# Kernel tuning notes

Hardware: AMD Instinct MI355X
Metric: run time of the kernel (lower is better)

Reference implementation:

```python
import jax, jax.numpy as jnp
import numpy as np

N0 = 1373      # hardcoded node-type split in the original forward
TAO = 0.4
EPS = 1e-12


def _l2norm(x, axis):
    # matches torch F.normalize(p=2): x / max(||x||, eps)
    n = jnp.sqrt(jnp.sum(x * x, axis=axis, keepdims=True))
    return x / jnp.maximum(n, EPS)


def setup_inputs() -> dict:
    key = jax.random.key(0)
    ks = jax.random.split(key, 12)
    N, E, D_IN, F, H, D = 20000, 320000, 256, 32, 8, 32
    feat = jax.random.normal(ks[0], (N, D_IN), jnp.float32)
    sloc = jax.random.normal(ks[1], (N, D), jnp.float32)
    topo_fea = jax.random.normal(ks[2], (N, D), jnp.float32)
    src = jax.random.randint(ks[3], (E,), 0, N)
    dst = jax.random.randint(ks[4], (E,), 0, N)
    e_feat = jax.random.randint(ks[5], (E,), 0, 4)
    s = 1.0 / np.sqrt(D_IN)
    W_proj0 = jax.random.normal(ks[6], (D_IN, H * F), jnp.float32) * s
    W_proj1 = jax.random.normal(ks[7], (D_IN, H * F), jnp.float32) * s
    W_prob = jax.random.normal(ks[8], (H, F, F), jnp.float32) * (1.0 / np.sqrt(F))
    W_res0 = jax.random.normal(ks[9], (D_IN, H * F), jnp.float32) * s
    W_res1 = jax.random.normal(ks[10], (D_IN, H * F), jnp.float32) * s
    etype_attn = jnp.ones((4,), jnp.float32)
    return dict(feat=feat, sloc=sloc, topo_fea=topo_fea, src=src, dst=dst,
                e_feat=e_feat, W_proj0=W_proj0, W_proj1=W_proj1, W_prob=W_prob,
                W_res0=W_res0, W_res1=W_res1, etype_attn=etype_attn)


def reference(feat, sloc, topo_fea, src, dst, e_feat,
              W_proj0, W_proj1, W_prob, W_res0, W_res1, etype_attn):
    N = feat.shape[0]
    H, F = W_prob.shape[0], W_prob.shape[2]
    sloc3 = sloc[:, None, :]        # (N,1,D) -- .unsqueeze(1)
    topo3 = topo_fea[:, None, :]

    # per-type node projection
    feat_src = jnp.concatenate(
        [feat[:N0] @ W_proj0, feat[N0:] @ W_proj1], axis=0).reshape(N, H, F)
    # per-head attention feature: softmax(tanh(fc4prob_i(.)), dim=feat)
    ft_attn = jax.nn.softmax(
        jnp.tanh(jnp.einsum('nhf,hfg->nhg', feat_src, W_prob)), axis=2)
    # F.normalize over the NODE dimension (dim=0), as in original
    ft_norm = _l2norm(feat_src, axis=0)

    sloc_n = _l2norm(sloc3, axis=2)
    topo_n = _l2norm(topo3, axis=2)

    # edge attention scores
    a = jnp.sum(ft_attn[dst] * ft_norm[src], axis=2, keepdims=True)   # (E,H,1)
    cos_s = jnp.sum(sloc_n[src] * sloc_n[dst], axis=2, keepdims=True)  # (E,1,1)
    cos_t = jnp.sum(topo_n[src] * topo_n[dst], axis=2, keepdims=True)
    sim = (TAO * cos_s + (1.0 - TAO) * cos_t + 1.0) / 2.0             # (E,1,1)
    e = (sim * a * etype_attn[e_feat][:, None, None])[:, :, 0]        # (E,H)

    # edge softmax: segment softmax over incoming edges of each dst node
    m = jax.ops.segment_max(e, dst, num_segments=N)                   # (N,H)
    ex = jnp.exp(e - m[dst])
    z = jax.ops.segment_sum(ex, dst, num_segments=N)
    att = ex / z[dst]                                                 # (E,H)

    # three u_mul_e + sum aggregations
    aw = att[:, :, None]                                              # (E,H,1)
    rst = jax.ops.segment_sum(feat_src[src] * aw, dst, num_segments=N)  # (N,H,F)
    sl2 = jax.ops.segment_sum(sloc3[src] * aw, dst, num_segments=N)     # (N,H,D)
    tp2 = jax.ops.segment_sum(topo3[src] * aw, dst, num_segments=N)     # (N,H,D)

    resval = jnp.concatenate(
        [feat[:N0] @ W_res0, feat[N0:] @ W_res1], axis=0).reshape(N, H, F)
    out_fea = jax.nn.relu(rst + resval).mean(axis=1)   # (N,F)
    out_sloc = (sl2 + sloc3).mean(axis=1)              # (N,D)
    out_topo = (tp2 + topo3).mean(axis=1)              # (N,D)
    return out_fea, out_sloc, out_topo
```

## Files before the change

kernel.cpp:

```cpp
#include <hip/hip_runtime.h>
#include <math.h>

#define HN0 1373
#define BM 128
#define BN 128
#define BK 32
#define LDT 40

typedef __attribute__((ext_vector_type(8))) short short8;
typedef __attribute__((ext_vector_type(4))) float f32x4;

__device__ inline unsigned short f2bf(float f) {
  unsigned int u = __float_as_uint(f);
  unsigned int r = (u + 0x7FFFu + ((u >> 16) & 1u)) >> 16;
  return (unsigned short)r;
}
__device__ inline float bflo(unsigned int u) { return __uint_as_float(u << 16); }
__device__ inline float bfhi(unsigned int u) { return __uint_as_float(u & 0xFFFF0000u); }

__device__ inline uint4 pack8bf(float4 a, float4 b) {
  uint4 o;
  o.x = (unsigned)f2bf(a.x) | ((unsigned)f2bf(a.y) << 16);
  o.y = (unsigned)f2bf(a.z) | ((unsigned)f2bf(a.w) << 16);
  o.z = (unsigned)f2bf(b.x) | ((unsigned)f2bf(b.y) << 16);
  o.w = (unsigned)f2bf(b.z) | ((unsigned)f2bf(b.w) << 16);
  return o;
}

__global__ __launch_bounds__(256) void prep(
    const float* __restrict__ Wp0, const float* __restrict__ Wr0,
    const float* __restrict__ Wp1, const float* __restrict__ Wr1,
    unsigned short* __restrict__ BTw,
    const float* __restrict__ sloc, const float* __restrict__ topo,
    float* __restrict__ inv_s, float* __restrict__ inv_t,
    unsigned short* __restrict__ slt,
    const int* __restrict__ dst, int* __restrict__ deg, int N, int E) {
  int b = blockIdx.x;
  int tid = threadIdx.x;
  int nodeBlocks = (N + 7) / 8;
  if (b < 1024) {
    int n = b & 511, g = b >> 9;
    const float* W;
    if (g == 0) W = (n < 256) ? Wp0 : Wr0;
    else        W = (n < 256) ? Wp1 : Wr1;
    int c = n & 255;
    BTw[(size_t)g * 512 * 256 + (size_t)n * 256 + tid] = f2bf(W[(size_t)tid * 256 + c]);
  } else if (b < 1024 + nodeBlocks) {
    int node = (b - 1024) * 8 + (tid >> 5);
    int d = tid & 31;
    if (node >= N) return;
    float s = sloc[(size_t)node * 32 + d];
    float t = topo[(size_t)node * 32 + d];
    float ss = s * s, tt = t * t;
#pragma unroll
    for (int m = 16; m >= 1; m >>= 1) {
      ss += __shfl_xor(ss, m);
      tt += __shfl_xor(tt, m);
    }
    if (d == 0) {
      inv_s[node] = 1.f / fmaxf(sqrtf(ss), 1e-12f);
      inv_t[node] = 1.f / fmaxf(sqrtf(tt), 1e-12f);
    }
    slt[(size_t)node * 64 + d] = f2bf(s);
    slt[(size_t)node * 64 + 32 + d] = f2bf(t);
  } else {
    int e = (b - 1024 - nodeBlocks) * 256 + tid;
    if (e < E) atomicAdd(&deg[dst[e]], 1);
  }
}

__global__ __launch_bounds__(256) void gemm_mfma(
    const float* __restrict__ A, const unsigned short* __restrict__ BTw,
    unsigned short* __restrict__ feat_bf, unsigned short* __restrict__ resval,
    int N) {
  __shared__ __align__(16) unsigned short As[BM * LDT];
  __shared__ __align__(16) unsigned short Bs[BN * LDT];
  int tid = threadIdx.x;
  int lane = tid & 63;
  int w = tid >> 6;
  int wr = w >> 1, wc = w & 1;

  int g0t = (HN0 + BM - 1) / BM;
  int bx = blockIdx.x;
  bool g1 = bx >= g0t;
  int rowBase = g1 ? HN0 + (bx - g0t) * BM : bx * BM;
  int rowEnd = g1 ? N : HN0;
  const unsigned short* BT = BTw + (g1 ? (size_t)512 * 256 : 0);
  int colBase = blockIdx.y * BN;

  int r0 = tid >> 2;
  int kp = (tid & 3) << 3;
  int ar1 = min(rowBase + r0, rowEnd - 1);
  int ar2 = min(rowBase + r0 + 64, rowEnd - 1);
  const float* aP1 = A + (size_t)ar1 * 256 + kp;
  const float* aP2 = A + (size_t)ar2 * 256 + kp;
  const unsigned short* bP1 = BT + (size_t)(colBase + r0) * 256 + kp;
  const unsigned short* bP2 = bP1 + (size_t)64 * 256;
  int wo1 = r0 * LDT + kp;
  int wo2 = (r0 + 64) * LDT + kp;

  int q = lane >> 4;
  int fr = lane & 15;
  int aOff = (wr * 64 + fr) * LDT + q * 8;
  int bOff = (wc * 64 + fr) * LDT + q * 8;

  f32x4 acc[4][4] = {};

  float4 fa1a = *reinterpret_cast<const float4*>(aP1);
  float4 fa1b = *reinterpret_cast<const float4*>(aP1 + 4);
  float4 fa2a = *reinterpret_cast<const float4*>(aP2);
  float4 fa2b = *reinterpret_cast<const float4*>(aP2 + 4);
  uint4 rb1 = *reinterpret_cast<const uint4*>(bP1);
  uint4 rb2 = *reinterpret_cast<const uint4*>(bP2);

  for (int t = 0; t < 8; ++t) {
    *reinterpret_cast<uint4*>(&As[wo1]) = pack8bf(fa1a, fa1b);
    *reinterpret_cast<uint4*>(&As[wo2]) = pack8bf(fa2a, fa2b);
    *reinterpret_cast<uint4*>(&Bs[wo1]) = rb1;
    *reinterpret_cast<uint4*>(&Bs[wo2]) = rb2;
    __syncthreads();
    if (t < 7) {
      int ko = (t + 1) * BK;
      fa1a = *reinterpret_cast<const float4*>(aP1 + ko);
      fa1b = *reinterpret_cast<const float4*>(aP1 + ko + 4);
      fa2a = *reinterpret_cast<const float4*>(aP2 + ko);
      fa2b = *reinterpret_cast<const float4*>(aP2 + ko + 4);
      rb1 = *reinterpret_cast<const uint4*>(bP1 + ko);
      rb2 = *reinterpret_cast<const uint4*>(bP2 + ko);
    }
    short8 af[4], bf4[4];
#pragma unroll
    for (int i = 0; i < 4; ++i) {
      af[i] = *reinterpret_cast<const short8*>(&As[aOff + i * 16 * LDT]);
      bf4[i] = *reinterpret_cast<const short8*>(&Bs[bOff + i * 16 * LDT]);
    }
#pragma unroll
    for (int i = 0; i < 4; ++i)
#pragma unroll
      for (int j = 0; j < 4; ++j)
        acc[i][j] = __builtin_amdgcn_mfma_f32_16x16x32_bf16(af[i], bf4[j], acc[i][j], 0, 0, 0);
    __syncthreads();
  }

  unsigned short* outp = (colBase < 256) ? feat_bf : resval;
  int cOff = colBase & 255;
#pragma unroll
  for (int i = 0; i < 4; ++i) {
    int rb = rowBase + wr * 64 + i * 16 + q * 4;
#pragma unroll
    for (int j = 0; j < 4; ++j) {
      int col = cOff + wc * 64 + j * 16 + fr;
      f32x4 v = acc[i][j];
#pragma unroll
      for (int rr = 0; rr < 4; ++rr) {
        int r = rb + rr;
        if (r < rowEnd) outp[(size_t)r * 256 + col] = f2bf(v[rr]);
      }
    }
  }
}

__global__ __launch_bounds__(256) void attn_probs(
    const unsigned short* __restrict__ feat_bf, const float* __restrict__ W_prob,
    unsigned short* __restrict__ ft_attn, float* __restrict__ col_ss, int N) {
  __shared__ float WL[8192];
  __shared__ float fsL[16 * 256];
  int tid = threadIdx.x;
  for (int i = tid; i < 8192; i += 256) WL[i] = W_prob[i];
  int nodeBase = blockIdx.x * 16;
  float ssp = 0.f;
  for (int i = 0; i < 16; ++i) {
    int n = nodeBase + i;
    float v = (n < N) ? __uint_as_float((unsigned)feat_bf[(size_t)n * 256 + tid] << 16) : 0.f;
    fsL[i * 256 + tid] = v;
    ssp += v * v;
  }
  atomicAdd(&col_ss[tid], ssp);
  __syncthreads();
  int h = tid >> 5, g = tid & 31;
  for (int i = 0; i < 16; ++i) {
    int n = nodeBase + i;
    if (n >= N) break;
    float t = 0.f;
    const float* wp = &WL[h * 1024 + g];
    const float* fr = &fsL[i * 256 + h * 32];
#pragma unroll
    for (int f = 0; f < 32; ++f) t = fmaf(fr[f], wp[f * 32], t);
    t = tanhf(t);
    float mx = t;
#pragma unroll
    for (int s = 16; s >= 1; s >>= 1) mx = fmaxf(mx, __shfl_xor(mx, s));
    float ex = __expf(t - mx);
    float sm = ex;
#pragma unroll
    for (int s = 16; s >= 1; s >>= 1) sm += __shfl_xor(sm, s);
    ft_attn[(size_t)n * 256 + tid] = f2bf(ex / sm);
  }
}

__global__ __launch_bounds__(512) void scan_block(const int* __restrict__ deg,
                                                  int* __restrict__ start,
                                                  int* __restrict__ bsum, int n) {
  __shared__ int buf[512];
  int tid = threadIdx.x;
  int gid = blockIdx.x * 512 + tid;
  int v = (gid < n) ? deg[gid] : 0;
  buf[tid] = v;
  __syncthreads();
  for (int off = 1; off < 512; off <<= 1) {
    int t = (tid >= off) ? buf[tid - off] : 0;
    __syncthreads();
    buf[tid] += t;
    __syncthreads();
  }
  if (gid < n) start[gid] = buf[tid] - v;
  if (tid == 511) bsum[blockIdx.x] = buf[511];
}

__global__ __launch_bounds__(256) void mid_small(float* __restrict__ col_ss,
                                                 int* __restrict__ bsum, int nb) {
  int tid = threadIdx.x;
  col_ss[tid] = 1.f / fmaxf(sqrtf(col_ss[tid]), 1e-12f);
  __shared__ int buf[128];
  if (tid < nb) buf[tid] = bsum[tid];
  __syncthreads();
  if (tid == 0) {
    int run = 0;
    for (int i = 0; i < nb; ++i) { int v = buf[i]; buf[i] = run; run += v; }
  }
  __syncthreads();
  if (tid < nb) bsum[tid] = buf[tid];
}

__global__ __launch_bounds__(256) void fill_sim(
    const int* __restrict__ src, const int* __restrict__ dst,
    const int* __restrict__ e_feat, const float* __restrict__ etype_attn,
    const unsigned short* __restrict__ slt,
    const float* __restrict__ inv_s, const float* __restrict__ inv_t,
    const int* __restrict__ start, const int* __restrict__ bsum,
    int* __restrict__ cursor, int2* __restrict__ csr, int E) {
  int tid = threadIdx.x;
  int j = tid & 7;
  int e = blockIdx.x * 32 + (tid >> 3);
  if (e >= E) return;
  int s = src[e], d = dst[e];
  const unsigned short* ps = slt + (size_t)s * 64 + j * 4;
  const unsigned short* pd = slt + (size_t)d * 64 + j * 4;
  uint2 sa = *reinterpret_cast<const uint2*>(ps);
  uint2 sb = *reinterpret_cast<const uint2*>(pd);
  uint2 ta = *reinterpret_cast<const uint2*>(ps + 32);
  uint2 tb = *reinterpret_cast<const uint2*>(pd + 32);
  float cs = bflo(sa.x) * bflo(sb.x) + bfhi(sa.x) * bfhi(sb.x) +
             bflo(sa.y) * bflo(sb.y) + bfhi(sa.y) * bfhi(sb.y);
  float ct = bflo(ta.x) * bflo(tb.x) + bfhi(ta.x) * bfhi(tb.x) +
             bflo(ta.y) * bflo(tb.y) + bfhi(ta.y) * bfhi(tb.y);
#pragma unroll
  for (int m = 4; m >= 1; m >>= 1) {
    cs += __shfl_xor(cs, m);
    ct += __shfl_xor(ct, m);
  }
  if (j == 0) {
    cs *= inv_s[s] * inv_s[d];
    ct *= inv_t[s] * inv_t[d];
    float sim = (0.4f * cs + 0.6f * ct + 1.f) * 0.5f;
    float wv = sim * etype_attn[e_feat[e]];
    int pos = start[d] + bsum[d >> 9] + atomicAdd(&cursor[d], 1);
    csr[pos] = make_int2(s, __float_as_int(wv));
  }
}

#define LOADIDX(K, V, W)                                                       \
  do {                                                                         \
    int2 c_ = csr[s0 + (K)];                                                   \
    V = c_.x;                                                                  \
    W = __int_as_float(c_.y);                                                  \
  } while (0)

#define GATHER(V, FP, SL, TP)                                                  \
  do {                                                                         \
    FP = *reinterpret_cast<const uint2*>(feat_bf + (size_t)(V) * 256 + fb);    \
    const unsigned short* sp_ = slt + (size_t)(V) * 64 + db;                   \
    SL = *reinterpret_cast<const uint2*>(sp_);                                 \
    TP = *reinterpret_cast<const uint2*>(sp_ + 32);                            \
  } while (0)

#define CONSUME(W, FP, SL, TP)                                                 \
  do {                                                                         \
    float fs0 = bflo(FP.x), fs1 = bfhi(FP.x);                                  \
    float fs2 = bflo(FP.y), fs3 = bfhi(FP.y);                                  \
    float pa = ai4.x * fs0 + ai4.y * fs1 + ai4.z * fs2 + ai4.w * fs3;          \
    pa += __shfl_xor(pa, 1);                                                   \
    pa += __shfl_xor(pa, 2);                                                   \
    pa += __shfl_xor(pa, 4);                                                   \
    float p = __expf(pa * (W));                                                \
    l += p;                                                                    \
    accf.x = fmaf(p, fs0, accf.x); accf.y = fmaf(p, fs1, accf.y);              \
    accf.z = fmaf(p, fs2, accf.z); accf.w = fmaf(p, fs3, accf.w);              \
    accs.x = fmaf(p, bflo(SL.x), accs.x); accs.y = fmaf(p, bfhi(SL.x), accs.y);\
    accs.z = fmaf(p, bflo(SL.y), accs.z); accs.w = fmaf(p, bfhi(SL.y), accs.w);\
    acct.x = fmaf(p, bflo(TP.x), acct.x); acct.y = fmaf(p, bfhi(TP.x), acct.y);\
    acct.z = fmaf(p, bflo(TP.y), acct.z); acct.w = fmaf(p, bfhi(TP.y), acct.w);\
  } while (0)

__global__ __launch_bounds__(128) void edge_aggregate(
    const unsigned short* __restrict__ feat_bf, const unsigned short* __restrict__ resval,
    const unsigned short* __restrict__ ft_attn, const float* __restrict__ inv_cn,
    const unsigned short* __restrict__ slt,
    const float* __restrict__ sloc, const float* __restrict__ topo,
    const int* __restrict__ start, const int* __restrict__ bsum,
    const int* __restrict__ deg, const int2* __restrict__ csr,
    float* __restrict__ out, int N) {
  int wave = threadIdx.x >> 6;
  int n = blockIdx.x * 2 + wave;
  if (n >= N) return;
  int lane = threadIdx.x & 63;
  int j = lane & 7;
  int fb = (lane >> 3) * 32 + j * 4;
  int db = j * 4;

  uint2 at2 = *reinterpret_cast<const uint2*>(ft_attn + (size_t)n * 256 + fb);
  float4 icn4 = *reinterpret_cast<const float4*>(inv_cn + fb);
  float4 ai4 = make_float4(bflo(at2.x) * icn4.x, bfhi(at2.x) * icn4.y,
                           bflo(at2.y) * icn4.z, bfhi(at2.y) * icn4.w);
  float l = 0.f;
  float4 accf = make_float4(0.f, 0.f, 0.f, 0.f);
  float4 accs = make_float4(0.f, 0.f, 0.f, 0.f);
  float4 acct = make_float4(0.f, 0.f, 0.f, 0.f);
  int s0 = start[n] + bsum[n >> 9];
  int dg = deg[n];

  int vA = 0, vB = 0, vC = 0;
  float wA = 0.f, wB = 0.f, wC = 0.f;
  uint2 fpA = make_uint2(0u, 0u), fpB = make_uint2(0u, 0u), fpC = make_uint2(0u, 0u);
  uint2 slA = make_uint2(0u, 0u), slB = make_uint2(0u, 0u), slC = make_uint2(0u, 0u);
  uint2 tpA = make_uint2(0u, 0u), tpB = make_uint2(0u, 0u), tpC = make_uint2(0u, 0u);
  if (dg > 0) { LOADIDX(0, vA, wA); GATHER(vA, fpA, slA, tpA); }
  if (dg > 1) { LOADIDX(1, vB, wB); GATHER(vB, fpB, slB, tpB); }
  if (dg > 2) { LOADIDX(2, vC, wC); GATHER(vC, fpC, slC, tpC); }
  int i = 0;
  for (; i + 2 < dg; i += 3) {
    CONSUME(wA, fpA, slA, tpA);
    if (i + 3 < dg) { LOADIDX(i + 3, vA, wA); GATHER(vA, fpA, slA, tpA); }
    CONSUME(wB, fpB, slB, tpB);
    if (i + 4 < dg) { LOADIDX(i + 4, vB, wB); GATHER(vB, fpB, slB, tpB); }
    CONSUME(wC, fpC, slC, tpC);
    if (i + 5 < dg) { LOADIDX(i + 5, vC, wC); GATHER(vC, fpC, slC, tpC); }
  }
  if (i < dg) CONSUME(wA, fpA, slA, tpA);
  if (i + 1 < dg) CONSUME(wB, fpB, slB, tpB);

  float invl = (l > 0.f) ? 1.f / l : 0.f;

  uint2 res2 = *reinterpret_cast<const uint2*>(resval + (size_t)n * 256 + fb);
  float4 of = make_float4(fmaxf(fmaf(accf.x, invl, bflo(res2.x)), 0.f),
                          fmaxf(fmaf(accf.y, invl, bfhi(res2.x)), 0.f),
                          fmaxf(fmaf(accf.z, invl, bflo(res2.y)), 0.f),
                          fmaxf(fmaf(accf.w, invl, bfhi(res2.y)), 0.f));
  float4 os = make_float4(accs.x * invl, accs.y * invl, accs.z * invl, accs.w * invl);
  float4 ot = make_float4(acct.x * invl, acct.y * invl, acct.z * invl, acct.w * invl);
#pragma unroll
  for (int msk = 8; msk <= 32; msk <<= 1) {
    of.x += __shfl_xor(of.x, msk); of.y += __shfl_xor(of.y, msk);
    of.z += __shfl_xor(of.z, msk); of.w += __shfl_xor(of.w, msk);
    os.x += __shfl_xor(os.x, msk); os.y += __shfl_xor(os.y, msk);
    os.z += __shfl_xor(os.z, msk); os.w += __shfl_xor(os.w, msk);
    ot.x += __shfl_xor(ot.x, msk); ot.y += __shfl_xor(ot.y, msk);
    ot.z += __shfl_xor(ot.z, msk); ot.w += __shfl_xor(ot.w, msk);
  }
  if (lane < 8) {
    float4 sln = *reinterpret_cast<const float4*>(sloc + (size_t)n * 32 + db);
    float4 tpn = *reinterpret_cast<const float4*>(topo + (size_t)n * 32 + db);
    float4 o0 = make_float4(of.x * 0.125f, of.y * 0.125f, of.z * 0.125f, of.w * 0.125f);
    float4 o1 = make_float4(fmaf(os.x, 0.125f, sln.x), fmaf(os.y, 0.125f, sln.y),
                            fmaf(os.z, 0.125f, sln.z), fmaf(os.w, 0.125f, sln.w));
    float4 o2 = make_float4(fmaf(ot.x, 0.125f, tpn.x), fmaf(ot.y, 0.125f, tpn.y),
                            fmaf(ot.z, 0.125f, tpn.z), fmaf(ot.w, 0.125f, tpn.w));
    *reinterpret_cast<float4*>(out + (size_t)n * 32 + db) = o0;
    *reinterpret_cast<float4*>(out + (size_t)N * 32 + (size_t)n * 32 + db) = o1;
    *reinterpret_cast<float4*>(out + (size_t)2 * N * 32 + (size_t)n * 32 + db) = o2;
  }
}

extern "C" void kernel_launch(void* const* d_in, const int* in_sizes, int n_in,
                              void* d_out, int out_size, void* d_ws, size_t ws_size,
                              hipStream_t stream) {
  const float* feat = (const float*)d_in[0];
  const float* sloc = (const float*)d_in[1];
  const float* topo = (const float*)d_in[2];
  const int* src = (const int*)d_in[3];
  const int* dst = (const int*)d_in[4];
  const int* e_feat = (const int*)d_in[5];
  const float* W_proj0 = (const float*)d_in[6];
  const float* W_proj1 = (const float*)d_in[7];
  const float* W_prob = (const float*)d_in[8];
  const float* W_res0 = (const float*)d_in[9];
  const float* W_res1 = (const float*)d_in[10];
  const float* etype_attn = (const float*)d_in[11];
  int E = in_sizes[3];
  int N = in_sizes[1] / 32;
  float* out = (float*)d_out;

  char* ws = (char*)d_ws;
  size_t off = 0;
  auto alloc = [&](size_t bytes) -> char* {
    char* p = ws + off;
    off += (bytes + 255) & ~(size_t)255;
    return p;
  };
  int* deg = (int*)alloc((size_t)N * 4);
  int* cursor = (int*)alloc((size_t)N * 4);
  float* col_ss = (float*)alloc(256 * 4);
  size_t zeroBytes = ((char*)col_ss + 256 * 4) - (char*)deg;
  int* startArr = (int*)alloc(((size_t)N + 1) * 4);
  int* bsum = (int*)alloc(128 * 4);
  float* inv_s = (float*)alloc((size_t)N * 4);
  float* inv_t = (float*)alloc((size_t)N * 4);
  int2* csr = (int2*)alloc((size_t)E * 8);
  unsigned short* feat_bf = (unsigned short*)alloc((size_t)N * 256 * 2);
  unsigned short* slt = (unsigned short*)alloc((size_t)N * 64 * 2);
  unsigned short* resval = (unsigned short*)alloc((size_t)N * 256 * 2);
  unsigned short* ft_attn = (unsigned short*)alloc((size_t)N * 256 * 2);
  unsigned short* BTw = (unsigned short*)alloc((size_t)2 * 512 * 256 * 2);

  hipMemsetAsync(deg, 0, zeroBytes, stream);

  int nodeBlocks = (N + 7) / 8;
  int degBlocks = (E + 255) / 256;
  prep<<<1024 + nodeBlocks + degBlocks, 256, 0, stream>>>(
      W_proj0, W_res0, W_proj1, W_res1, BTw, sloc, topo, inv_s, inv_t, slt,
      dst, deg, N, E);

  int g0t = (HN0 + BM - 1) / BM;
  int g1t = (N - HN0 + BM - 1) / BM;
  gemm_mfma<<<dim3(g0t + g1t, 4), 256, 0, stream>>>(feat, BTw, feat_bf, resval, N);

  attn_probs<<<(N + 15) / 16, 256, 0, stream>>>(feat_bf, W_prob, ft_attn, col_ss, N);

  int nb = (N + 511) / 512;
  scan_block<<<nb, 512, 0, stream>>>(deg, startArr, bsum, N);
  mid_small<<<1, 256, 0, stream>>>(col_ss, bsum, nb);

  fill_sim<<<(E + 31) / 32, 256, 0, stream>>>(src, dst, e_feat, etype_attn, slt,
                                              inv_s, inv_t, startArr, bsum,
                                              cursor, csr, E);

  edge_aggregate<<<(N + 1) / 2, 128, 0, stream>>>(feat_bf, resval, ft_attn, col_ss,
                                                  slt, sloc, topo, startArr, bsum,
                                                  deg, csr, out, N);
}
```

Before: 190.2 us.

## Tile weight transpose, prenormalize sloc/topo, register W_prob, cheaper tanh softmax

The weight transpose in prep now uses 64x64 shared-memory tiles with vectorized loads and stores, replacing 1024 blocks of strided scalar reads. Prep also writes pre-normalized bf16 sloc/topo (sltn), so fill_sim only does a weighted dot product over 16-wide vector loads with four lanes per edge and no inv_s/inv_t gathers. attn_probs keeps W_prob in registers instead of shared memory. It computes tanh through exp and a fast reciprocal, and drops the max subtraction because tanh output is bounded. These trade extra bf16 rounding of normalized values and approximate tanh and reciprocal for fewer memory passes and less arithmetic.

```diff
diff --git a/kernel.cpp b/kernel.cpp
--- a/kernel.cpp
+++ b/kernel.cpp
@@ -32,21 +32,46 @@
     const float* __restrict__ Wp1, const float* __restrict__ Wr1,
     unsigned short* __restrict__ BTw,
     const float* __restrict__ sloc, const float* __restrict__ topo,
-    float* __restrict__ inv_s, float* __restrict__ inv_t,
-    unsigned short* __restrict__ slt,
+    unsigned short* __restrict__ slt, unsigned short* __restrict__ sltn,
     const int* __restrict__ dst, int* __restrict__ deg, int N, int E) {
+  __shared__ float T[64][72];
   int b = blockIdx.x;
   int tid = threadIdx.x;
   int nodeBlocks = (N + 7) / 8;
-  if (b < 1024) {
-    int n = b & 511, g = b >> 9;
-    const float* W;
-    if (g == 0) W = (n < 256) ? Wp0 : Wr0;
-    else        W = (n < 256) ? Wp1 : Wr1;
-    int c = n & 255;
-    BTw[(size_t)g * 512 * 256 + (size_t)n * 256 + tid] = f2bf(W[(size_t)tid * 256 + c]);
-  } else if (b < 1024 + nodeBlocks) {
-    int node = (b - 1024) * 8 + (tid >> 5);
+  if (b < 64) {
+    int mat = b >> 4;
+    int t16 = b & 15;
+    int kT = (t16 & 3) * 64;
+    int nT = (t16 >> 2) * 64;
+    const float* W = (mat == 0) ? Wp0 : (mat == 1) ? Wr0 : (mat == 2) ? Wp1 : Wr1;
+    int g = mat >> 1;
+    int nbase = (mat & 1) * 256;
+    int r = tid >> 2;
+    int cb = (tid & 3) * 16;
+    const float* srcp = W + (size_t)(kT + r) * 256 + nT + cb;
+#pragma unroll
+    for (int q = 0; q < 4; ++q) {
+      float4 v = *reinterpret_cast<const float4*>(srcp + q * 4);
+      T[cb + q * 4 + 0][r] = v.x;
+      T[cb + q * 4 + 1][r] = v.y;
+      T[cb + q * 4 + 2][r] = v.z;
+      T[cb + q * 4 + 3][r] = v.w;
+    }
+    __syncthreads();
+    int nl = tid >> 2;
+    int kb = (tid & 3) * 16;
+    unsigned int pk[8];
+#pragma unroll
+    for (int q = 0; q < 8; ++q) {
+      unsigned short lo = f2bf(T[nl][kb + q * 2]);
+      unsigned short hi = f2bf(T[nl][kb + q * 2 + 1]);
+      pk[q] = (unsigned)lo | ((unsigned)hi << 16);
+    }
+    unsigned short* dstp = BTw + (size_t)g * 512 * 256 + (size_t)(nbase + nT + nl) * 256 + kT + kb;
+    *reinterpret_cast<uint4*>(dstp) = make_uint4(pk[0], pk[1], pk[2], pk[3]);
+    *reinterpret_cast<uint4*>(dstp + 8) = make_uint4(pk[4], pk[5], pk[6], pk[7]);
+  } else if (b < 64 + nodeBlocks) {
+    int node = (b - 64) * 8 + (tid >> 5);
     int d = tid & 31;
     if (node >= N) return;
     float s = sloc[(size_t)node * 32 + d];
@@ -57,14 +82,14 @@
       ss += __shfl_xor(ss, m);
       tt += __shfl_xor(tt, m);
     }
-    if (d == 0) {
-      inv_s[node] = 1.f / fmaxf(sqrtf(ss), 1e-12f);
-      inv_t[node] = 1.f / fmaxf(sqrtf(tt), 1e-12f);
-    }
+    float is = 1.f / fmaxf(sqrtf(ss), 1e-12f);
+    float it = 1.f / fmaxf(sqrtf(tt), 1e-12f);
     slt[(size_t)node * 64 + d] = f2bf(s);
     slt[(size_t)node * 64 + 32 + d] = f2bf(t);
+    sltn[(size_t)node * 64 + d] = f2bf(s * is);
+    sltn[(size_t)node * 64 + 32 + d] = f2bf(t * it);
   } else {
-    int e = (b - 1024 - nodeBlocks) * 256 + tid;
+    int e = (b - 64 - nodeBlocks) * 256 + tid;
     if (e < E) atomicAdd(&deg[dst[e]], 1);
   }
 }
@@ -163,10 +188,12 @@
 __global__ __launch_bounds__(256) void attn_probs(
     const unsigned short* __restrict__ feat_bf, const float* __restrict__ W_prob,
     unsigned short* __restrict__ ft_attn, float* __restrict__ col_ss, int N) {
-  __shared__ float WL[8192];
   __shared__ float fsL[16 * 256];
   int tid = threadIdx.x;
-  for (int i = tid; i < 8192; i += 256) WL[i] = W_prob[i];
+  int h = tid >> 5, g = tid & 31;
+  float wreg[32];
+#pragma unroll
+  for (int f = 0; f < 32; ++f) wreg[f] = W_prob[h * 1024 + f * 32 + g];
   int nodeBase = blockIdx.x * 16;
   float ssp = 0.f;
   for (int i = 0; i < 16; ++i) {
@@ -177,24 +204,20 @@
   }
   atomicAdd(&col_ss[tid], ssp);
   __syncthreads();
-  int h = tid >> 5, g = tid & 31;
   for (int i = 0; i < 16; ++i) {
     int n = nodeBase + i;
     if (n >= N) break;
+    const float* fr = &fsL[i * 256 + h * 32];
     float t = 0.f;
-    const float* wp = &WL[h * 1024 + g];
-    const float* fr = &fsL[i * 256 + h * 32];
-#pragma unroll
-    for (int f = 0; f < 32; ++f) t = fmaf(fr[f], wp[f * 32], t);
-    t = tanhf(t);
-    float mx = t;
-#pragma unroll
-    for (int s = 16; s >= 1; s >>= 1) mx = fmaxf(mx, __shfl_xor(mx, s));
-    float ex = __expf(t - mx);
+#pragma unroll
+    for (int f = 0; f < 32; ++f) t = fmaf(fr[f], wreg[f], t);
+    float e2 = __expf(2.f * t);
+    t = 1.f - 2.f * __builtin_amdgcn_rcpf(e2 + 1.f);
+    float ex = __expf(t);
     float sm = ex;
 #pragma unroll
     for (int s = 16; s >= 1; s >>= 1) sm += __shfl_xor(sm, s);
-    ft_attn[(size_t)n * 256 + tid] = f2bf(ex / sm);
+    ft_attn[(size_t)n * 256 + tid] = f2bf(ex * __builtin_amdgcn_rcpf(sm));
   }
 }
 
@@ -235,34 +258,33 @@
 __global__ __launch_bounds__(256) void fill_sim(
     const int* __restrict__ src, const int* __restrict__ dst,
     const int* __restrict__ e_feat, const float* __restrict__ etype_attn,
-    const unsigned short* __restrict__ slt,
-    const float* __restrict__ inv_s, const float* __restrict__ inv_t,
+    const unsigned short* __restrict__ sltn,
     const int* __restrict__ start, const int* __restrict__ bsum,
     int* __restrict__ cursor, int2* __restrict__ csr, int E) {
   int tid = threadIdx.x;
-  int j = tid & 7;
-  int e = blockIdx.x * 32 + (tid >> 3);
+  int j = tid & 3;
+  int e = blockIdx.x * 64 + (tid >> 2);
   if (e >= E) return;
   int s = src[e], d = dst[e];
-  const unsigned short* ps = slt + (size_t)s * 64 + j * 4;
-  const unsigned short* pd = slt + (size_t)d * 64 + j * 4;
-  uint2 sa = *reinterpret_cast<const uint2*>(ps);
-  uint2 sb = *reinterpret_cast<const uint2*>(pd);
-  uint2 ta = *reinterpret_cast<const uint2*>(ps + 32);
-  uint2 tb = *reinterpret_cast<const uint2*>(pd + 32);
-  float cs = bflo(sa.x) * bflo(sb.x) + bfhi(sa.x) * bfhi(sb.x) +
-             bflo(sa.y) * bflo(sb.y) + bfhi(sa.y) * bfhi(sb.y);
-  float ct = bflo(ta.x) * bflo(tb.x) + bfhi(ta.x) * bfhi(tb.x) +
-             bflo(ta.y) * bflo(tb.y) + bfhi(ta.y) * bfhi(tb.y);
-#pragma unroll
-  for (int m = 4; m >= 1; m >>= 1) {
-    cs += __shfl_xor(cs, m);
-    ct += __shfl_xor(ct, m);
-  }
+  const unsigned short* ps = sltn + (size_t)s * 64 + j * 16;
+  const unsigned short* pd = sltn + (size_t)d * 64 + j * 16;
+  uint4 a0 = *reinterpret_cast<const uint4*>(ps);
+  uint4 a1 = *reinterpret_cast<const uint4*>(ps + 8);
+  uint4 b0 = *reinterpret_cast<const uint4*>(pd);
+  uint4 b1 = *reinterpret_cast<const uint4*>(pd + 8);
+  float u = bflo(a0.x) * bflo(b0.x) + bfhi(a0.x) * bfhi(b0.x) +
+            bflo(a0.y) * bflo(b0.y) + bfhi(a0.y) * bfhi(b0.y) +
+            bflo(a0.z) * bflo(b0.z) + bfhi(a0.z) * bfhi(b0.z) +
+            bflo(a0.w) * bflo(b0.w) + bfhi(a0.w) * bfhi(b0.w) +
+            bflo(a1.x) * bflo(b1.x) + bfhi(a1.x) * bfhi(b1.x) +
+            bflo(a1.y) * bflo(b1.y) + bfhi(a1.y) * bfhi(b1.y) +
+            bflo(a1.z) * bflo(b1.z) + bfhi(a1.z) * bfhi(b1.z) +
+            bflo(a1.w) * bflo(b1.w) + bfhi(a1.w) * bfhi(b1.w);
+  u *= (j < 2) ? 0.4f : 0.6f;
+  u += __shfl_xor(u, 1);
+  u += __shfl_xor(u, 2);
   if (j == 0) {
-    cs *= inv_s[s] * inv_s[d];
-    ct *= inv_t[s] * inv_t[d];
-    float sim = (0.4f * cs + 0.6f * ct + 1.f) * 0.5f;
+    float sim = fmaf(u, 0.5f, 0.5f);
     float wv = sim * etype_attn[e_feat[e]];
     int pos = start[d] + bsum[d >> 9] + atomicAdd(&cursor[d], 1);
     csr[pos] = make_int2(s, __float_as_int(wv));
@@ -365,7 +387,7 @@
     os.x += __shfl_xor(os.x, msk); os.y += __shfl_xor(os.y, msk);
     os.z += __shfl_xor(os.z, msk); os.w += __shfl_xor(os.w, msk);
     ot.x += __shfl_xor(ot.x, msk); ot.y += __shfl_xor(ot.y, msk);
-    ot.z += __shfl_xor(ot.z, msk); ot.w += __shfl_xor(ot.w, msk);
+    ot.w += __shfl_xor(ot.w, msk); ot.z += __shfl_xor(ot.z, msk);
   }
   if (lane < 8) {
     float4 sln = *reinterpret_cast<const float4*>(sloc + (size_t)n * 32 + db);
@@ -413,11 +435,10 @@
   size_t zeroBytes = ((char*)col_ss + 256 * 4) - (char*)deg;
   int* startArr = (int*)alloc(((size_t)N + 1) * 4);
   int* bsum = (int*)alloc(128 * 4);
-  float* inv_s = (float*)alloc((size_t)N * 4);
-  float* inv_t = (float*)alloc((size_t)N * 4);
   int2* csr = (int2*)alloc((size_t)E * 8);
   unsigned short* feat_bf = (unsigned short*)alloc((size_t)N * 256 * 2);
   unsigned short* slt = (unsigned short*)alloc((size_t)N * 64 * 2);
+  unsigned short* sltn = (unsigned short*)alloc((size_t)N * 64 * 2);
   unsigned short* resval = (unsigned short*)alloc((size_t)N * 256 * 2);
   unsigned short* ft_attn = (unsigned short*)alloc((size_t)N * 256 * 2);
   unsigned short* BTw = (unsigned short*)alloc((size_t)2 * 512 * 256 * 2);
@@ -426,9 +447,8 @@
 
   int nodeBlocks = (N + 7) / 8;
   int degBlocks = (E + 255) / 256;
-  prep<<<1024 + nodeBlocks + degBlocks, 256, 0, stream>>>(
-      W_proj0, W_res0, W_proj1, W_res1, BTw, sloc, topo, inv_s, inv_t, slt,
-      dst, deg, N, E);
+  prep<<<64 + nodeBlocks + degBlocks, 256, 0, stream>>>(
+      W_proj0, W_res0, W_proj1, W_res1, BTw, sloc, topo, slt, sltn, dst, deg, N, E);
 
   int g0t = (HN0 + BM - 1) / BM;
   int g1t = (N - HN0 + BM - 1) / BM;
@@ -440,9 +460,8 @@
   scan_block<<<nb, 512, 0, stream>>>(deg, startArr, bsum, N);
   mid_small<<<1, 256, 0, stream>>>(col_ss, bsum, nb);
 
-  fill_sim<<<(E + 31) / 32, 256, 0, stream>>>(src, dst, e_feat, etype_attn, slt,
-                                              inv_s, inv_t, startArr, bsum,
-                                              cursor, csr, E);
+  fill_sim<<<(E + 63) / 64, 256, 0, stream>>>(src, dst, e_feat, etype_attn, sltn,
+                                              startArr, bsum, cursor, csr, E);
 
   edge_aggregate<<<(N + 1) / 2, 128, 0, stream>>>(feat_bf, resval, ft_attn, col_ss,
                                                   slt, sloc, topo, startArr, bsum,
```

After: 178.2 us. 6.3% less time.
